# Optimization experiments

Measured on AMD Instinct MI355X. Metric: run time of the kernel, lower is better.

## Reference

```python
import jax, jax.numpy as jnp
import numpy as np


def _three_nn_interp(xyz1, xyz2, feat2):
    # squared Euclidean distances via gram trick, avoids (B,N,S,3) tensor
    # d2: (B, N, S)
    n1 = jnp.sum(xyz1 * xyz1, axis=-1)               # (B, N)
    n2 = jnp.sum(xyz2 * xyz2, axis=-1)               # (B, S)
    d2 = n1[:, :, None] + n2[:, None, :] - 2.0 * jnp.einsum('bnc,bsc->bns', xyz1, xyz2)
    d = jnp.sqrt(jnp.maximum(d2, 0.0))
    k = min(3, xyz2.shape[1])
    neg_d, idx = jax.lax.top_k(-d, k)                # smallest k distances
    dist = jnp.maximum(-neg_d, 1e-10)               # (B, N, k)
    w = 1.0 / dist
    w = w / jnp.sum(w, axis=-1, keepdims=True)
    # gather feat2 at idx: (B, N, k, C2)
    f2 = jnp.take_along_axis(feat2[:, None, :, :], idx[..., None], axis=2)
    return jnp.sum(f2 * w[..., None], axis=2)        # (B, N, C2)


def setup_inputs() -> dict:
    key = jax.random.key(0)
    ks = jax.random.split(key, 8)
    B, N, S, C1, C2, OUT = 8, 8192, 2048, 128, 256, 256
    IN = C1 + C2
    return {
        'xyz1': jax.random.normal(ks[0], (B, N, 3), dtype=jnp.float32),
        'xyz2': jax.random.normal(ks[1], (B, S, 3), dtype=jnp.float32),
        'feat1': jax.random.normal(ks[2], (B, N, C1), dtype=jnp.float32),
        'feat2': jax.random.normal(ks[3], (B, S, C2), dtype=jnp.float32),
        'W1': jax.random.normal(ks[4], (IN, OUT), dtype=jnp.float32) * (1.0 / np.sqrt(IN)),
        'b1': jnp.zeros((OUT,), dtype=jnp.float32),
        'W2': jax.random.normal(ks[5], (OUT, OUT), dtype=jnp.float32) * (1.0 / np.sqrt(OUT)),
        'b2': jnp.zeros((OUT,), dtype=jnp.float32),
    }


def reference(xyz1, xyz2, feat1, feat2, W1, b1, W2, b2):
    if xyz2.shape[1] == 1:
        interp = jnp.broadcast_to(feat2, (feat2.shape[0], xyz1.shape[1], feat2.shape[2]))
    else:
        interp = _three_nn_interp(xyz1, xyz2, feat2)
    x = jnp.concatenate([feat1, interp], axis=-1)    # (B, N, C1+C2)
    x = jax.nn.relu(x @ W1 + b1)
    x = jax.nn.relu(x @ W2 + b2)
    return x
```

## Files before the change

kernel.cpp:

```cpp
#include <hip/hip_runtime.h>
#include <hip/hip_bf16.h>

#define BB   8
#define NN   8192
#define SS   2048
#define C1C  128
#define C2C  256
#define KIN  384
#define OUTC 256

typedef __attribute__((ext_vector_type(4))) float f32x4;
typedef __attribute__((ext_vector_type(8))) short short8;
typedef __attribute__((ext_vector_type(8))) unsigned short ushortx8;

__device__ __forceinline__ ushort f2bf(float v) {
    __hip_bfloat16 h = __float2bfloat16(v);
    return __builtin_bit_cast(ushort, h);
}

__device__ __forceinline__ float med3(float a, float b, float c) {
    return __builtin_amdgcn_fmed3f(a, b, c);
}

__global__ __launch_bounds__(1024, 8) void knn_gather_prep_kernel(
    const float* __restrict__ xyz1, const float* __restrict__ xyz2,
    const float* __restrict__ feat2, ushort* __restrict__ interpB,
    const float* __restrict__ W1, ushort* __restrict__ W1t,
    const float* __restrict__ W2, ushort* __restrict__ W2pack)
{
    __shared__ float4 sp[SS];
    __shared__ int   sIdx[128][3];
    __shared__ float sW[128][3];

    const int tid   = threadIdx.x;
    const int b     = blockIdx.x & 7;
    const int chunk = blockIdx.x >> 3;
    const int qbase = chunk << 7;

    const float* x2 = xyz2 + (size_t)b * SS * 3;
    for (int i = tid; i < SS; i += 1024) {
        float x = x2[i*3+0], y = x2[i*3+1], z = x2[i*3+2];
        sp[i] = make_float4(-2.f*x, -2.f*y, -2.f*z, x*x + y*y + z*z);
    }

    {
        const int idx = blockIdx.x * 1024 + tid;
        const int n1 = KIN * OUTC;
        if (idx < n1) {
            int n = idx / KIN, k = idx - n * KIN;
            W1t[idx] = f2bf(W1[(size_t)k * OUTC + n]);
        } else if (idx < n1 + OUTC * OUTC) {
            int o = idx - n1;
            int e = o & 7, lane = (o >> 3) & 63, j = (o >> 9) & 3;
            int wc = (o >> 11) & 3, s = o >> 13;
            int n = wc * 64 + j * 16 + (lane & 15);
            int k = s * 32 + (lane >> 4) * 8 + e;
            W2pack[o] = f2bf(W2[(size_t)k * OUTC + n]);
        }
    }
    __syncthreads();

    const int g = tid >> 4;
    const int l = tid & 15;
    const int qa = qbase + g * 2;

    const float* qp = xyz1 + ((size_t)b * NN + qa) * 3;
    float px[2] = {qp[0], qp[3]};
    float py[2] = {qp[1], qp[4]};
    float pz[2] = {qp[2], qp[5]};

    float c0[2], c1[2], c2[2];
#pragma unroll
    for (int qi = 0; qi < 2; ++qi) { c0[qi] = c1[qi] = c2[qi] = 1e30f; }

    for (int jj = 0; jj < 128; jj += 4) {
        float4 P[4];
#pragma unroll
        for (int u = 0; u < 4; ++u) P[u] = sp[((jj + u) << 4) + l];
#pragma unroll
        for (int u = 0; u < 4; ++u) {
#pragma unroll
            for (int qi = 0; qi < 2; ++qi) {
                float f = fmaf(px[qi], P[u].x,
                          fmaf(py[qi], P[u].y,
                          fmaf(pz[qi], P[u].z, P[u].w)));
                c2[qi] = med3(f, c1[qi], c2[qi]);
                c1[qi] = med3(f, c0[qi], c1[qi]);
                c0[qi] = fminf(f, c0[qi]);
            }
        }
    }

#pragma unroll
    for (int m = 1; m <= 8; m <<= 1) {
#pragma unroll
        for (int qi = 0; qi < 2; ++qi) {
            float b0 = __shfl_xor(c0[qi], m);
            float b1 = __shfl_xor(c1[qi], m);
            float b2 = __shfl_xor(c2[qi], m);
            float bv[3] = {b0, b1, b2};
#pragma unroll
            for (int e = 0; e < 3; ++e) {
                float d = bv[e];
                c2[qi] = med3(d, c1[qi], c2[qi]);
                c1[qi] = med3(d, c0[qi], c1[qi]);
                c0[qi] = fminf(d, c0[qi]);
            }
        }
    }
    const float t0 = c2[0], t1 = c2[1];

    float e0[2], e1[2], e2[2];
    int   i0[2], i1[2], i2[2];
#pragma unroll
    for (int qi = 0; qi < 2; ++qi) {
        e0[qi] = e1[qi] = e2[qi] = 1e30f;
        i0[qi] = i1[qi] = i2[qi] = 0x3fffffff;
    }

    for (int jj = 0; jj < 128; jj += 4) {
        float4 P[4];
#pragma unroll
        for (int u = 0; u < 4; ++u) P[u] = sp[((jj + u) << 4) + l];
#pragma unroll
        for (int u = 0; u < 4; ++u) {
            const int s = ((jj + u) << 4) + l;
#pragma unroll
            for (int qi = 0; qi < 2; ++qi) {
                float f = fmaf(px[qi], P[u].x,
                          fmaf(py[qi], P[u].y,
                          fmaf(pz[qi], P[u].z, P[u].w)));
                float tq = qi ? t1 : t0;
                if (f <= tq) {
                    bool lt2 = (f < e2[qi]) || (f == e2[qi] && s < i2[qi]);
                    if (lt2) {
                        bool lt1 = (f < e1[qi]) || (f == e1[qi] && s < i1[qi]);
                        bool lt0 = (f < e0[qi]) || (f == e0[qi] && s < i0[qi]);
                        e2[qi] = lt1 ? e1[qi] : f;  i2[qi] = lt1 ? i1[qi] : s;
                        e1[qi] = lt0 ? e0[qi] : (lt1 ? f : e1[qi]);
                        i1[qi] = lt0 ? i0[qi] : (lt1 ? s : i1[qi]);
                        e0[qi] = lt0 ? f : e0[qi];  i0[qi] = lt0 ? s : i0[qi];
                    }
                }
            }
        }
    }

#pragma unroll
    for (int m = 1; m <= 8; m <<= 1) {
#pragma unroll
        for (int qi = 0; qi < 2; ++qi) {
            float ob0 = __shfl_xor(e0[qi], m), ob1 = __shfl_xor(e1[qi], m), ob2 = __shfl_xor(e2[qi], m);
            int   oj0 = __shfl_xor(i0[qi], m), oj1 = __shfl_xor(i1[qi], m), oj2 = __shfl_xor(i2[qi], m);
            float dv[3] = {ob0, ob1, ob2}; int iv[3] = {oj0, oj1, oj2};
#pragma unroll
            for (int e = 0; e < 3; ++e) {
                float d = dv[e]; int s = iv[e];
                bool lt2 = (d < e2[qi]) || (d == e2[qi] && s < i2[qi]);
                if (lt2) {
                    bool lt1 = (d < e1[qi]) || (d == e1[qi] && s < i1[qi]);
                    bool lt0 = (d < e0[qi]) || (d == e0[qi] && s < i0[qi]);
                    e2[qi] = lt1 ? e1[qi] : d;  i2[qi] = lt1 ? i1[qi] : s;
                    e1[qi] = lt0 ? e0[qi] : (lt1 ? d : e1[qi]);
                    i1[qi] = lt0 ? i0[qi] : (lt1 ? s : i1[qi]);
                    e0[qi] = lt0 ? d : e0[qi];  i0[qi] = lt0 ? s : i0[qi];
                }
            }
        }
    }

    if (l == 0) {
#pragma unroll
        for (int qi = 0; qi < 2; ++qi) {
            float nx = px[qi], ny = py[qi], nz = pz[qi];
            float n1 = nx*nx + ny*ny + nz*nz;
            float d0 = sqrtf(fmaxf(n1 + e0[qi], 0.f));
            float d1 = sqrtf(fmaxf(n1 + e1[qi], 0.f));
            float d2s = sqrtf(fmaxf(n1 + e2[qi], 0.f));
            float w0 = 1.f / fmaxf(d0, 1e-10f);
            float w1 = 1.f / fmaxf(d1, 1e-10f);
            float w2 = 1.f / fmaxf(d2s, 1e-10f);
            float wsum = w0 + w1 + w2;
            int qq = g * 2 + qi;
            sIdx[qq][0] = i0[qi]; sIdx[qq][1] = i1[qi]; sIdx[qq][2] = i2[qi];
            sW[qq][0] = w0 / wsum; sW[qq][1] = w1 / wsum; sW[qq][2] = w2 / wsum;
        }
    }
    __syncthreads();

    const int wid = tid >> 6, lane = tid & 63;
    for (int qq = wid; qq < 128; qq += 16) {
        int a0 = sIdx[qq][0], a1 = sIdx[qq][1], a2 = sIdx[qq][2];
        float w0 = sW[qq][0], w1 = sW[qq][1], w2 = sW[qq][2];
        const float4* r0 = (const float4*)(feat2 + ((size_t)b * SS + a0) * C2C);
        const float4* r1 = (const float4*)(feat2 + ((size_t)b * SS + a1) * C2C);
        const float4* r2 = (const float4*)(feat2 + ((size_t)b * SS + a2) * C2C);
        float4 v0 = r0[lane], v1 = r1[lane], v2 = r2[lane];
        ushort4 o;
        o.x = f2bf(w0*v0.x + w1*v1.x + w2*v2.x);
        o.y = f2bf(w0*v0.y + w1*v1.y + w2*v2.y);
        o.z = f2bf(w0*v0.z + w1*v1.z + w2*v2.z);
        o.w = f2bf(w0*v0.w + w1*v1.w + w2*v2.w);
        *(ushort4*)(interpB + ((size_t)b * NN + qbase + qq) * C2C + lane * 4) = o;
    }
}

#define GBM 128
#define GBN 256
#define GBK 32

__device__ __forceinline__ void gld_lds16(const void* g, void* l) {
    __builtin_amdgcn_global_load_lds(
        (const __attribute__((address_space(1))) void*)g,
        (__attribute__((address_space(3))) void*)l, 16, 0, 0);
}

__global__ __launch_bounds__(512, 4) void gemm_fused(
    const float* __restrict__ feat1,
    const ushort* __restrict__ interpB,
    const ushort* __restrict__ W1t, const float* __restrict__ b1,
    const ushort* __restrict__ W2pack, const float* __restrict__ b2,
    float* __restrict__ out)
{
    __shared__ ushort pool[GBM * 256];

    const int tid  = threadIdx.x;
    const int lane = tid & 63;
    const int wid  = tid >> 6;
    const int m0   = blockIdx.x * GBM;
    const int wr   = wid >> 2;
    const int wc   = wid & 3;

    const int rsub = lane >> 2;
    const int slot = lane & 3;
    const int csub = slot * 8;
    const int usw  = (slot ^ (rsub & 3)) * 8;

    const int kgrp = (lane >> 4) * 8;
    const int rl   = lane & 15;
    const int ksw  = kgrp ^ ((rl & 3) << 3);
    const int cl   = lane & 15;
    const int rgrp = (lane >> 4) * 4;

    auto stageAB = [&](int k0, int buf) {
        ushort* sAb = pool + buf * 12288;
        ushort* sBb = sAb + 4096;
#pragma unroll
        for (int c = 0; c < 3; ++c) {
            const int cid = wid * 3 + c;
            if (cid < 8) {
                const int r = m0 + cid * 16 + rsub;
                if (k0 < C1C) {
                    const float* src = feat1 + (size_t)r * C1C + k0 + usw;
                    float4 u = ((const float4*)src)[0];
                    float4 v = ((const float4*)src)[1];
                    ushortx8 t;
                    t[0] = f2bf(u.x); t[1] = f2bf(u.y); t[2] = f2bf(u.z); t[3] = f2bf(u.w);
                    t[4] = f2bf(v.x); t[5] = f2bf(v.y); t[6] = f2bf(v.z); t[7] = f2bf(v.w);
                    *(ushortx8*)&sAb[cid * 512 + rsub * 32 + csub] = t;
                } else {
                    gld_lds16(interpB + (size_t)r * C2C + (k0 - C1C) + usw, &sAb[cid * 512]);
                }
            } else {
                const int bi = cid - 8;
                const int r = bi * 16 + rsub;
                gld_lds16(W1t + (size_t)r * KIN + k0 + usw, &sBb[bi * 512]);
            }
        }
    };

    f32x4 acc1[4][4];
#pragma unroll
    for (int i = 0; i < 4; ++i)
#pragma unroll
        for (int j = 0; j < 4; ++j) acc1[i][j] = (f32x4){0.f, 0.f, 0.f, 0.f};

    int cur = 0;
    stageAB(0, 0);
    for (int k0 = 0; k0 < KIN; k0 += GBK) {
        __syncthreads();
        if (k0 + GBK < KIN) stageAB(k0 + GBK, cur ^ 1);

        const ushort* sAb = pool + cur * 12288;
        const ushort* sBb = sAb + 4096;
        short8 af[4], bf[4];
#pragma unroll
        for (int i = 0; i < 4; ++i) {
            af[i] = *(const short8*)&sAb[(wr * 64 + i * 16 + rl) * GBK + ksw];
            bf[i] = *(const short8*)&sBb[(wc * 64 + i * 16 + rl) * GBK + ksw];
        }
#pragma unroll
        for (int i = 0; i < 4; ++i)
#pragma unroll
            for (int j = 0; j < 4; ++j)
                acc1[i][j] = __builtin_amdgcn_mfma_f32_16x16x32_bf16(
                    af[i], bf[j], acc1[i][j], 0, 0, 0);
        cur ^= 1;
    }
    __syncthreads();

    short8 bfc[4], bfn[4];
#pragma unroll
    for (int j = 0; j < 4; ++j)
        bfc[j] = *(const short8*)&W2pack[(size_t)(0 * 16 + wc * 4 + j) * 512 + lane * 8];

#pragma unroll
    for (int j = 0; j < 4; ++j) {
        const int c = wc * 64 + j * 16 + cl;
        const float bv = b1[c];
        const int u = c >> 3, sub = c & 7;
#pragma unroll
        for (int i = 0; i < 4; ++i) {
#pragma unroll
            for (int rr = 0; rr < 4; ++rr) {
                const int r = wr * 64 + i * 16 + rgrp + rr;
                const float v = fmaxf(acc1[i][j][rr] + bv, 0.f);
                pool[r * 256 + ((u ^ (r & 31)) << 3) + sub] = f2bf(v);
            }
        }
    }
    __syncthreads();

    f32x4 acc2[4][4];
#pragma unroll
    for (int i = 0; i < 4; ++i)
#pragma unroll
        for (int j = 0; j < 4; ++j) acc2[i][j] = (f32x4){0.f, 0.f, 0.f, 0.f};

    for (int s = 0; s < 8; ++s) {
        if (s < 7) {
#pragma unroll
            for (int j = 0; j < 4; ++j)
                bfn[j] = *(const short8*)&W2pack[(size_t)((s + 1) * 16 + wc * 4 + j) * 512 + lane * 8];
        }
        const int ub = s * 4 + (lane >> 4);
        short8 af[4];
#pragma unroll
        for (int i = 0; i < 4; ++i) {
            const int r = wr * 64 + i * 16 + rl;
            af[i] = *(const short8*)&pool[r * 256 + ((ub ^ (r & 31)) << 3)];
        }
#pragma unroll
        for (int i = 0; i < 4; ++i)
#pragma unroll
            for (int j = 0; j < 4; ++j)
                acc2[i][j] = __builtin_amdgcn_mfma_f32_16x16x32_bf16(
                    af[i], bfc[j], acc2[i][j], 0, 0, 0);
#pragma unroll
        for (int j = 0; j < 4; ++j) bfc[j] = bfn[j];
    }

#pragma unroll
    for (int j = 0; j < 4; ++j) {
        const int col = wc * 64 + j * 16 + cl;
        const float bv = b2[col];
#pragma unroll
        for (int i = 0; i < 4; ++i) {
            const int rowb = m0 + wr * 64 + i * 16 + rgrp;
#pragma unroll
            for (int rr = 0; rr < 4; ++rr) {
                out[(size_t)(rowb + rr) * OUTC + col] =
                    fmaxf(acc2[i][j][rr] + bv, 0.f);
            }
        }
    }
}

extern "C" void kernel_launch(void* const* d_in, const int* in_sizes, int n_in,
                              void* d_out, int out_size, void* d_ws, size_t ws_size,
                              hipStream_t stream) {
    const float* xyz1  = (const float*)d_in[0];
    const float* xyz2  = (const float*)d_in[1];
    const float* feat1 = (const float*)d_in[2];
    const float* feat2 = (const float*)d_in[3];
    const float* W1    = (const float*)d_in[4];
    const float* b1    = (const float*)d_in[5];
    const float* W2    = (const float*)d_in[6];
    const float* b2    = (const float*)d_in[7];
    float* out = (float*)d_out;

    char* ws = (char*)d_ws;
    ushort* interpB = (ushort*)(ws);
    ushort* W1t     = (ushort*)(ws + 33554432);
    ushort* W2pack  = (ushort*)(ws + 33751040);

    const int M = BB * NN;

    knn_gather_prep_kernel<<<512, 1024, 0, stream>>>(xyz1, xyz2, feat2, interpB,
                                                     W1, W1t, W2, W2pack);

    gemm_fused<<<M / GBM, 512, 0, stream>>>(feat1, interpB,
                                            W1t, b1, W2pack, b2, out);
}
```

Measured before the change: 102.0 us.

## Load W1 fragments directly from pre-packed global layout instead of LDS staging

```diff
diff --git a/kernel.cpp b/kernel.cpp
--- a/kernel.cpp
+++ b/kernel.cpp
@@ -25,7 +25,7 @@
 __global__ __launch_bounds__(1024, 8) void knn_gather_prep_kernel(
     const float* __restrict__ xyz1, const float* __restrict__ xyz2,
     const float* __restrict__ feat2, ushort* __restrict__ interpB,
-    const float* __restrict__ W1, ushort* __restrict__ W1t,
+    const float* __restrict__ W1, ushort* __restrict__ W1pack,
     const float* __restrict__ W2, ushort* __restrict__ W2pack)
 {
     __shared__ float4 sp[SS];
@@ -45,10 +45,14 @@
 
     {
         const int idx = blockIdx.x * 1024 + tid;
-        const int n1 = KIN * OUTC;
+        const int n1 = 12 * 16 * 512;
         if (idx < n1) {
-            int n = idx / KIN, k = idx - n * KIN;
-            W1t[idx] = f2bf(W1[(size_t)k * OUTC + n]);
+            int o = idx;
+            int e = o & 7, lane = (o >> 3) & 63, j = (o >> 9) & 3;
+            int wc = (o >> 11) & 3, s = o >> 13;
+            int n = wc * 64 + j * 16 + (lane & 15);
+            int k = s * 32 + (lane >> 4) * 8 + e;
+            W1pack[o] = f2bf(W1[(size_t)k * OUTC + n]);
         } else if (idx < n1 + OUTC * OUTC) {
             int o = idx - n1;
             int e = o & 7, lane = (o >> 3) & 63, j = (o >> 9) & 3;
@@ -218,7 +222,7 @@
 __global__ __launch_bounds__(512, 4) void gemm_fused(
     const float* __restrict__ feat1,
     const ushort* __restrict__ interpB,
-    const ushort* __restrict__ W1t, const float* __restrict__ b1,
+    const ushort* __restrict__ W1pack, const float* __restrict__ b1,
     const ushort* __restrict__ W2pack, const float* __restrict__ b2,
     float* __restrict__ out)
 {
@@ -242,30 +246,19 @@
     const int cl   = lane & 15;
     const int rgrp = (lane >> 4) * 4;
 
-    auto stageAB = [&](int k0, int buf) {
-        ushort* sAb = pool + buf * 12288;
-        ushort* sBb = sAb + 4096;
-#pragma unroll
-        for (int c = 0; c < 3; ++c) {
-            const int cid = wid * 3 + c;
-            if (cid < 8) {
-                const int r = m0 + cid * 16 + rsub;
-                if (k0 < C1C) {
-                    const float* src = feat1 + (size_t)r * C1C + k0 + usw;
-                    float4 u = ((const float4*)src)[0];
-                    float4 v = ((const float4*)src)[1];
-                    ushortx8 t;
-                    t[0] = f2bf(u.x); t[1] = f2bf(u.y); t[2] = f2bf(u.z); t[3] = f2bf(u.w);
-                    t[4] = f2bf(v.x); t[5] = f2bf(v.y); t[6] = f2bf(v.z); t[7] = f2bf(v.w);
-                    *(ushortx8*)&sAb[cid * 512 + rsub * 32 + csub] = t;
-                } else {
-                    gld_lds16(interpB + (size_t)r * C2C + (k0 - C1C) + usw, &sAb[cid * 512]);
-                }
-            } else {
-                const int bi = cid - 8;
-                const int r = bi * 16 + rsub;
-                gld_lds16(W1t + (size_t)r * KIN + k0 + usw, &sBb[bi * 512]);
-            }
+    auto stageA = [&](int k0, int buf) {
+        ushort* sAb = pool + buf * 4096;
+        const int r = m0 + wid * 16 + rsub;
+        if (k0 < C1C) {
+            const float* src = feat1 + (size_t)r * C1C + k0 + usw;
+            float4 u = ((const float4*)src)[0];
+            float4 v = ((const float4*)src)[1];
+            ushortx8 t;
+            t[0] = f2bf(u.x); t[1] = f2bf(u.y); t[2] = f2bf(u.z); t[3] = f2bf(u.w);
+            t[4] = f2bf(v.x); t[5] = f2bf(v.y); t[6] = f2bf(v.z); t[7] = f2bf(v.w);
+            *(ushortx8*)&sAb[wid * 512 + rsub * 32 + csub] = t;
+        } else {
+            gld_lds16(interpB + (size_t)r * C2C + (k0 - C1C) + usw, &sAb[wid * 512]);
         }
     };
 
@@ -276,30 +269,38 @@
         for (int j = 0; j < 4; ++j) acc1[i][j] = (f32x4){0.f, 0.f, 0.f, 0.f};
 
     int cur = 0;
-    stageAB(0, 0);
-    for (int k0 = 0; k0 < KIN; k0 += GBK) {
+    stageA(0, 0);
+    short8 bfc[4], bfn[4];
+#pragma unroll
+    for (int j = 0; j < 4; ++j)
+        bfc[j] = *(const short8*)&W1pack[(size_t)(0 * 16 + wc * 4 + j) * 512 + lane * 8];
+
+    for (int k0 = 0, s = 0; k0 < KIN; k0 += GBK, ++s) {
         __syncthreads();
-        if (k0 + GBK < KIN) stageAB(k0 + GBK, cur ^ 1);
-
-        const ushort* sAb = pool + cur * 12288;
-        const ushort* sBb = sAb + 4096;
-        short8 af[4], bf[4];
-#pragma unroll
-        for (int i = 0; i < 4; ++i) {
+        if (k0 + GBK < KIN) {
+            stageA(k0 + GBK, cur ^ 1);
+#pragma unroll
+            for (int j = 0; j < 4; ++j)
+                bfn[j] = *(const short8*)&W1pack[(size_t)((s + 1) * 16 + wc * 4 + j) * 512 + lane * 8];
+        }
+
+        const ushort* sAb = pool + cur * 4096;
+        short8 af[4];
+#pragma unroll
+        for (int i = 0; i < 4; ++i)
             af[i] = *(const short8*)&sAb[(wr * 64 + i * 16 + rl) * GBK + ksw];
-            bf[i] = *(const short8*)&sBb[(wc * 64 + i * 16 + rl) * GBK + ksw];
-        }
 #pragma unroll
         for (int i = 0; i < 4; ++i)
 #pragma unroll
             for (int j = 0; j < 4; ++j)
                 acc1[i][j] = __builtin_amdgcn_mfma_f32_16x16x32_bf16(
-                    af[i], bf[j], acc1[i][j], 0, 0, 0);
+                    af[i], bfc[j], acc1[i][j], 0, 0, 0);
+#pragma unroll
+        for (int j = 0; j < 4; ++j) bfc[j] = bfn[j];
         cur ^= 1;
     }
     __syncthreads();
 
-    short8 bfc[4], bfn[4];
 #pragma unroll
     for (int j = 0; j < 4; ++j)
         bfc[j] = *(const short8*)&W2pack[(size_t)(0 * 16 + wc * 4 + j) * 512 + lane * 8];
@@ -381,14 +382,14 @@
 
     char* ws = (char*)d_ws;
     ushort* interpB = (ushort*)(ws);
-    ushort* W1t     = (ushort*)(ws + 33554432);
+    ushort* W1pack  = (ushort*)(ws + 33554432);
     ushort* W2pack  = (ushort*)(ws + 33751040);
 
     const int M = BB * NN;
 
     knn_gather_prep_kernel<<<512, 1024, 0, stream>>>(xyz1, xyz2, feat2, interpB,
-                                                     W1, W1t, W2, W2pack);
+                                                     W1, W1pack, W2, W2pack);
 
     gemm_fused<<<M / GBM, 512, 0, stream>>>(feat1, interpB,
-                                            W1t, b1, W2pack, b2, out);
-}
+                                            W1pack, b1, W2pack, b2, out);
+}
```

After: 97.54 us (median of 2 runs). -4.4%, faster.
